# Kernel optimization log

Measured on AMD Instinct MI355X. Metric: run time of the kernel, lower is better.

## Reference

```python
import jax, jax.numpy as jnp
import numpy as np

N = 100000
E = 1600000
D = 64
BETA = 1.0


def setup_inputs() -> dict:
    key = jax.random.key(0)
    ks = jax.random.split(key, 6)
    x = jax.random.normal(ks[0], (N, D), dtype=jnp.float32)
    edge_index = jax.random.randint(ks[1], (2, E), 0, N, dtype=jnp.int64)
    s = 1.0 / np.sqrt(D)
    Wm = jax.random.uniform(ks[2], (D, D), jnp.float32, -s, s)
    bm = jax.random.uniform(ks[3], (D,), jnp.float32, -s, s)
    Wr = jax.random.uniform(ks[4], (D, D), jnp.float32, -s, s)
    br = jax.random.uniform(ks[5], (D,), jnp.float32, -s, s)
    return {"x": x, "edge_index": edge_index, "Wm": Wm, "bm": bm, "Wr": Wr, "br": br}


def reference(x, edge_index, Wm, bm, Wr, br):
    row, col = edge_index[0], edge_index[1]
    # gather source features and apply message linear: [E, D]
    messages = x[row] @ Wm + bm
    scores = BETA * messages.mean(axis=-1)  # [E]
    # edge softmax over incoming edges of each destination node (col)
    seg_max = jax.ops.segment_max(scores, col, num_segments=N)  # [N]
    ex = jnp.exp(scores - seg_max[col])  # [E]
    seg_sum = jax.ops.segment_sum(ex, col, num_segments=N)  # [N]
    weights = ex / seg_sum[col]  # [E]
    # weighted scatter-add back to destinations
    out = jax.ops.segment_sum(messages * weights[:, None], col, num_segments=N)
    return out + (x @ Wr + br)
```

## Files before the change

kernel.cpp:

```cpp
#include <hip/hip_runtime.h>
#include <math.h>

#define N_NODES 100000
#define DIM 64
#define N_EDGES 1600000

#define NBF 782
#define BK_NODES 128
#define CAP 3072

#define SC_CHUNK 8192
#define SC_BLOCKS ((N_EDGES + SC_CHUNK - 1) / SC_CHUNK)

#define HB 128
#define LIN_BLOCKS 1563
#define P1_BLOCKS (HB + LIN_BLOCKS)

typedef _Float16 half8 __attribute__((ext_vector_type(8)));
typedef _Float16 half4 __attribute__((ext_vector_type(4)));
typedef float f32x4 __attribute__((ext_vector_type(4)));

__global__ __launch_bounds__(256) void k_phase1(
        const float* __restrict__ x,
        const float* __restrict__ Wm, const float* __restrict__ bm,
        const float* __restrict__ Wr, const float* __restrict__ br,
        const int* __restrict__ col, int* __restrict__ hist,
        _Float16* __restrict__ Mh, float* __restrict__ es,
        float* __restrict__ out) {
    __shared__ int cnt[NBF];
    if (blockIdx.x < HB) {
        for (int i = threadIdx.x; i < NBF; i += 256) cnt[i] = 0;
        __syncthreads();
        for (int e = blockIdx.x * 256 + threadIdx.x; e < N_EDGES; e += HB * 256)
            atomicAdd(&cnt[col[e] >> 7], 1);
        __syncthreads();
        for (int i = threadIdx.x; i < NBF; i += 256)
            if (cnt[i]) atomicAdd(&hist[i], cnt[i]);
        return;
    }

    const int wave = (blockIdx.x - HB) * 4 + (threadIdx.x >> 6);
    if (wave >= N_NODES / 16) return;
    const int lane = threadIdx.x & 63;
    const int quad = lane >> 4;
    const int l15 = lane & 15;
    const int row0 = wave * 16;

    half8 bfrag[8][2];
#pragma unroll
    for (int ct = 0; ct < 8; ++ct) {
        const float* W = (ct < 4) ? Wm : Wr;
        const int c = (ct & 3) * 16 + l15;
#pragma unroll
        for (int kc = 0; kc < 2; ++kc) {
            half8 f;
#pragma unroll
            for (int j = 0; j < 8; ++j)
                f[j] = (_Float16)W[(kc * 32 + quad * 8 + j) * DIM + c];
            bfrag[ct][kc] = f;
        }
    }

    half8 afrag[2];
#pragma unroll
    for (int kc = 0; kc < 2; ++kc) {
        const float* xp = x + (size_t)(row0 + l15) * DIM + kc * 32 + quad * 8;
        const float4 x0 = *(const float4*)xp;
        const float4 x1 = *(const float4*)(xp + 4);
        half8 f;
        f[0] = (_Float16)x0.x; f[1] = (_Float16)x0.y;
        f[2] = (_Float16)x0.z; f[3] = (_Float16)x0.w;
        f[4] = (_Float16)x1.x; f[5] = (_Float16)x1.y;
        f[6] = (_Float16)x1.z; f[7] = (_Float16)x1.w;
        afrag[kc] = f;
    }

    f32x4 acc[8];
#pragma unroll
    for (int ct = 0; ct < 8; ++ct) {
        f32x4 a = {0.f, 0.f, 0.f, 0.f};
        a = __builtin_amdgcn_mfma_f32_16x16x32_f16(afrag[0], bfrag[ct][0], a, 0, 0, 0);
        a = __builtin_amdgcn_mfma_f32_16x16x32_f16(afrag[1], bfrag[ct][1], a, 0, 0, 0);
        acc[ct] = a;
    }

    float rsum[4] = {0.f, 0.f, 0.f, 0.f};
#pragma unroll
    for (int ct = 0; ct < 8; ++ct) {
        const float bias = (ct < 4) ? bm[(ct & 3) * 16 + l15]
                                    : br[(ct & 3) * 16 + l15];
#pragma unroll
        for (int r = 0; r < 4; ++r) {
            const float v = acc[ct][r] + bias;
            const size_t idx = (size_t)(row0 + quad * 4 + r) * DIM + (ct & 3) * 16 + l15;
            if (ct < 4) {
                Mh[idx] = (_Float16)v;
                rsum[r] += v;
            } else {
                out[idx] = v;
            }
        }
    }
#pragma unroll
    for (int o = 1; o <= 8; o <<= 1) {
#pragma unroll
        for (int r = 0; r < 4; ++r) rsum[r] += __shfl_xor(rsum[r], o, 64);
    }
    if (l15 == 0) {
#pragma unroll
        for (int r = 0; r < 4; ++r)
            es[row0 + quad * 4 + r] = __expf(rsum[r] * (1.0f / DIM));
    }
}


__global__ __launch_bounds__(1024) void k_scatter(
        const int* __restrict__ row, const int* __restrict__ col,
        int* __restrict__ cursor, unsigned int* __restrict__ pairs) {
    __shared__ int cnt[NBF];
    __shared__ int base_l[NBF];
    __shared__ int base_g[NBF];
    __shared__ int sd[1024];
    __shared__ unsigned int stage[SC_CHUNK];
    __shared__ unsigned short stage_bk[SC_CHUNK];

    const int t = threadIdx.x;
    const int start = blockIdx.x * SC_CHUNK;
    const int mEnd = min(N_EDGES, start + SC_CHUNK);

    for (int i = t; i < NBF; i += 1024) cnt[i] = 0;
    __syncthreads();

    int rr[8], cc[8], lr[8];
#pragma unroll
    for (int k = 0; k < 8; ++k) {
        const int idx = start + k * 1024 + t;
        if (idx < mEnd) {
            cc[k] = col[idx];
            rr[k] = row[idx];
            lr[k] = atomicAdd(&cnt[cc[k] >> 7], 1);
        }
    }
    __syncthreads();

    const int v = (t < NBF) ? cnt[t] : 0;
    sd[t] = v;
    __syncthreads();
    for (int o = 1; o < 1024; o <<= 1) {
        const int add = (t >= o) ? sd[t - o] : 0;
        __syncthreads();
        sd[t] += add;
        __syncthreads();
    }
    if (t < NBF) {
        base_l[t] = sd[t] - v;
        if (v > 0) base_g[t] = atomicAdd(&cursor[t], v);
    }
    __syncthreads();

#pragma unroll
    for (int k = 0; k < 8; ++k) {
        const int idx = start + k * 1024 + t;
        if (idx < mEnd) {
            const int bk = cc[k] >> 7;
            const int slot = base_l[bk] + lr[k];
            stage[slot] = ((unsigned int)rr[k] << 7) | (unsigned int)(cc[k] & 127);
            stage_bk[slot] = (unsigned short)bk;
        }
    }
    __syncthreads();

    const int m = mEnd - start;
    for (int i = t; i < m; i += 1024) {
        const int bk = stage_bk[i];
        const int gslot = base_g[bk] + (i - base_l[bk]);
        if (gslot < CAP) pairs[(size_t)bk * CAP + gslot] = stage[i];
    }
}

__global__ __launch_bounds__(512) void k_bucket_gather(
        const unsigned int* __restrict__ pairs, const int* __restrict__ cursor,
        const float* __restrict__ es, const half4* __restrict__ Mh4,
        float4* __restrict__ out4) {
    __shared__ unsigned int sorted[CAP];
    __shared__ int cnt[BK_NODES];
    __shared__ int off[BK_NODES];
    const int b = blockIdx.x;
    const int t = threadIdx.x;
    const int m = min(cursor[b], CAP);
    const size_t base = (size_t)b * CAP;

    if (t < BK_NODES) cnt[t] = 0;
    __syncthreads();

    unsigned int pk[6];
    int rk[6];
#pragma unroll
    for (int k = 0; k < 6; ++k) {
        const int i = k * 512 + t;
        if (i < m) {
            pk[k] = pairs[base + i];
            rk[k] = atomicAdd(&cnt[pk[k] & 127u], 1);
        }
    }
    __syncthreads();

    int v = 0;
    if (t < BK_NODES) {
        v = cnt[t];
        off[t] = v;
    }
    __syncthreads();
    for (int o = 1; o < BK_NODES; o <<= 1) {
        int add = 0;
        if (t < BK_NODES && t >= o) add = off[t - o];
        __syncthreads();
        if (t < BK_NODES) off[t] += add;
        __syncthreads();
    }
    if (t < BK_NODES) off[t] -= v;
    __syncthreads();

#pragma unroll
    for (int k = 0; k < 6; ++k) {
        const int i = k * 512 + t;
        if (i < m) sorted[off[pk[k] & 127u] + rk[k]] = pk[k];
    }
    __syncthreads();

    const int g = t >> 4;
    const int gl = t & 15;
    for (int c = g; c < BK_NODES; c += 32) {
        const int node = b * BK_NODES + c;
        if (node >= N_NODES) break;
        const int s0i = off[c];
        const int len = cnt[c];
        if (len == 0) continue;

        float a0x = 0.f, a0y = 0.f, a0z = 0.f, a0w = 0.f, l0 = 0.f;
        float a1x = 0.f, a1y = 0.f, a1z = 0.f, a1w = 0.f, l1 = 0.f;
        int j = 0;
        for (; j + 1 < len; j += 2) {
            const int s0 = (int)(sorted[s0i + j] >> 7);
            const int s1 = (int)(sorted[s0i + j + 1] >> 7);
            const float w0 = es[s0];
            const float w1 = es[s1];
            const half4 m0 = Mh4[(size_t)s0 * 16 + gl];
            const half4 m1 = Mh4[(size_t)s1 * 16 + gl];
            l0 += w0; l1 += w1;
            a0x = fmaf(w0, (float)m0[0], a0x); a0y = fmaf(w0, (float)m0[1], a0y);
            a0z = fmaf(w0, (float)m0[2], a0z); a0w = fmaf(w0, (float)m0[3], a0w);
            a1x = fmaf(w1, (float)m1[0], a1x); a1y = fmaf(w1, (float)m1[1], a1y);
            a1z = fmaf(w1, (float)m1[2], a1z); a1w = fmaf(w1, (float)m1[3], a1w);
        }
        if (j < len) {
            const int s0 = (int)(sorted[s0i + j] >> 7);
            const float w0 = es[s0];
            const half4 m0 = Mh4[(size_t)s0 * 16 + gl];
            l0 += w0;
            a0x = fmaf(w0, (float)m0[0], a0x); a0y = fmaf(w0, (float)m0[1], a0y);
            a0z = fmaf(w0, (float)m0[2], a0z); a0w = fmaf(w0, (float)m0[3], a0w);
        }
        const float inv = 1.0f / (l0 + l1);
        float4 r = out4[(size_t)node * 16 + gl];
        r.x = fmaf(a0x + a1x, inv, r.x);
        r.y = fmaf(a0y + a1y, inv, r.y);
        r.z = fmaf(a0z + a1z, inv, r.z);
        r.w = fmaf(a0w + a1w, inv, r.w);
        out4[(size_t)node * 16 + gl] = r;
    }
}

extern "C" void kernel_launch(void* const* d_in, const int* in_sizes, int n_in,
                              void* d_out, int out_size, void* d_ws, size_t ws_size,
                              hipStream_t stream) {
    const float* x  = (const float*)d_in[0];
    const int*   ei = (const int*)d_in[1];
    const float* Wm = (const float*)d_in[2];
    const float* bm = (const float*)d_in[3];
    const float* Wr = (const float*)d_in[4];
    const float* br = (const float*)d_in[5];
    float* out = (float*)d_out;
    const int* row = ei;
    const int* col = ei + N_EDGES;

    char* ws = (char*)d_ws;
    _Float16* Mh    = (_Float16*)ws;     ws += (size_t)N_NODES * DIM * sizeof(_Float16);
    float* es       = (float*)ws;        ws += (size_t)N_NODES * sizeof(float);
    int* hist       = (int*)ws;          ws += (size_t)1024 * sizeof(int);
    int* cursor     = (int*)ws;          ws += (size_t)1024 * sizeof(int);
    unsigned int* pairs = (unsigned int*)ws; ws += (size_t)NBF * CAP * sizeof(unsigned int);

    hipMemsetAsync(cursor, 0, NBF * sizeof(int), stream);

    k_phase1<<<P1_BLOCKS, 256, 0, stream>>>(x, Wm, bm, Wr, br,
                                            col, hist, Mh, es, out);
    k_scatter<<<SC_BLOCKS, 1024, 0, stream>>>(row, col, cursor, pairs);
    k_bucket_gather<<<NBF, 512, 0, stream>>>(pairs, cursor, es,
                                             (const half4*)Mh, (float4*)out);
}
```

Baseline: 164.7 us.

## Fuse edge scatter into GEMM phase kernel and drop unused histogram

Merges the edge bucket-scatter kernel into the node GEMM kernel as extra blocks of a single launch, so the scatter and the dense transform run at the same time and one launch is removed. The unused histogram pass is deleted. The shared-memory prefix scan is replaced by a wave-shuffle scan, which cuts the number of barriers. GEMM blocks now run 16 waves at 1024 threads and carry the large shared-memory footprint of the scatter path, which may lower occupancy for the GEMM part.

After: 157.3 us. -4.5%, faster.

```diff
diff --git a/kernel.cpp b/kernel.cpp
--- a/kernel.cpp
+++ b/kernel.cpp
@@ -12,36 +12,100 @@
 #define SC_CHUNK 8192
 #define SC_BLOCKS ((N_EDGES + SC_CHUNK - 1) / SC_CHUNK)
 
-#define HB 128
-#define LIN_BLOCKS 1563
-#define P1_BLOCKS (HB + LIN_BLOCKS)
+#define GEMM_BLOCKS ((N_NODES / 16 + 15) / 16)
+#define PH_BLOCKS (SC_BLOCKS + GEMM_BLOCKS)
 
 typedef _Float16 half8 __attribute__((ext_vector_type(8)));
 typedef _Float16 half4 __attribute__((ext_vector_type(4)));
 typedef float f32x4 __attribute__((ext_vector_type(4)));
 
-__global__ __launch_bounds__(256) void k_phase1(
+__global__ __launch_bounds__(1024) void k_phase(
         const float* __restrict__ x,
         const float* __restrict__ Wm, const float* __restrict__ bm,
         const float* __restrict__ Wr, const float* __restrict__ br,
-        const int* __restrict__ col, int* __restrict__ hist,
+        const int* __restrict__ row, const int* __restrict__ col,
+        int* __restrict__ cursor, unsigned int* __restrict__ pairs,
         _Float16* __restrict__ Mh, float* __restrict__ es,
         float* __restrict__ out) {
     __shared__ int cnt[NBF];
-    if (blockIdx.x < HB) {
-        for (int i = threadIdx.x; i < NBF; i += 256) cnt[i] = 0;
-        __syncthreads();
-        for (int e = blockIdx.x * 256 + threadIdx.x; e < N_EDGES; e += HB * 256)
-            atomicAdd(&cnt[col[e] >> 7], 1);
-        __syncthreads();
-        for (int i = threadIdx.x; i < NBF; i += 256)
-            if (cnt[i]) atomicAdd(&hist[i], cnt[i]);
+    __shared__ int base_l[NBF];
+    __shared__ int base_g[NBF];
+    __shared__ int wsum[16];
+    __shared__ unsigned int stage[SC_CHUNK];
+    __shared__ unsigned short stage_bk[SC_CHUNK];
+
+    const int t = threadIdx.x;
+    const int lane = t & 63;
+    const int wid = t >> 6;
+
+    if (blockIdx.x < SC_BLOCKS) {
+        const int start = blockIdx.x * SC_CHUNK;
+        const int mEnd = min(N_EDGES, start + SC_CHUNK);
+
+        for (int i = t; i < NBF; i += 1024) cnt[i] = 0;
+        __syncthreads();
+
+        int rr[8], cc[8], lr[8];
+#pragma unroll
+        for (int k = 0; k < 8; ++k) {
+            const int idx = start + k * 1024 + t;
+            if (idx < mEnd) {
+                cc[k] = col[idx];
+                rr[k] = row[idx];
+                lr[k] = atomicAdd(&cnt[cc[k] >> 7], 1);
+            }
+        }
+        __syncthreads();
+
+        const int v = (t < NBF) ? cnt[t] : 0;
+        int inc = v;
+#pragma unroll
+        for (int o = 1; o < 64; o <<= 1) {
+            const int u = __shfl_up(inc, o, 64);
+            if (lane >= o) inc += u;
+        }
+        if (lane == 63) wsum[wid] = inc;
+        __syncthreads();
+        if (wid == 0) {
+            const int wv = (lane < 16) ? wsum[lane] : 0;
+            int winc = wv;
+#pragma unroll
+            for (int o = 1; o < 16; o <<= 1) {
+                const int u = __shfl_up(winc, o, 64);
+                if (lane >= o) winc += u;
+            }
+            if (lane < 16) wsum[lane] = winc - wv;
+        }
+        __syncthreads();
+        if (t < NBF) {
+            base_l[t] = inc - v + wsum[wid];
+            if (v > 0) base_g[t] = atomicAdd(&cursor[t], v);
+        }
+        __syncthreads();
+
+#pragma unroll
+        for (int k = 0; k < 8; ++k) {
+            const int idx = start + k * 1024 + t;
+            if (idx < mEnd) {
+                const int bk = cc[k] >> 7;
+                const int slot = base_l[bk] + lr[k];
+                stage[slot] = ((unsigned int)rr[k] << 7) | (unsigned int)(cc[k] & 127);
+                stage_bk[slot] = (unsigned short)bk;
+            }
+        }
+        __syncthreads();
+
+        const int m = mEnd - start;
+        for (int i = t; i < m; i += 1024) {
+            const int bk = stage_bk[i];
+            const int gslot = base_g[bk] + (i - base_l[bk]);
+            if (gslot < CAP) pairs[(size_t)bk * CAP + gslot] = stage[i];
+        }
         return;
     }
 
-    const int wave = (blockIdx.x - HB) * 4 + (threadIdx.x >> 6);
+    const int wave = (blockIdx.x - SC_BLOCKS) * 16 + wid;
     if (wave >= N_NODES / 16) return;
-    const int lane = threadIdx.x & 63;
     const int quad = lane >> 4;
     const int l15 = lane & 15;
     const int row0 = wave * 16;
@@ -110,71 +174,6 @@
 #pragma unroll
         for (int r = 0; r < 4; ++r)
             es[row0 + quad * 4 + r] = __expf(rsum[r] * (1.0f / DIM));
-    }
-}
-
-
-__global__ __launch_bounds__(1024) void k_scatter(
-        const int* __restrict__ row, const int* __restrict__ col,
-        int* __restrict__ cursor, unsigned int* __restrict__ pairs) {
-    __shared__ int cnt[NBF];
-    __shared__ int base_l[NBF];
-    __shared__ int base_g[NBF];
-    __shared__ int sd[1024];
-    __shared__ unsigned int stage[SC_CHUNK];
-    __shared__ unsigned short stage_bk[SC_CHUNK];
-
-    const int t = threadIdx.x;
-    const int start = blockIdx.x * SC_CHUNK;
-    const int mEnd = min(N_EDGES, start + SC_CHUNK);
-
-    for (int i = t; i < NBF; i += 1024) cnt[i] = 0;
-    __syncthreads();
-
-    int rr[8], cc[8], lr[8];
-#pragma unroll
-    for (int k = 0; k < 8; ++k) {
-        const int idx = start + k * 1024 + t;
-        if (idx < mEnd) {
-            cc[k] = col[idx];
-            rr[k] = row[idx];
-            lr[k] = atomicAdd(&cnt[cc[k] >> 7], 1);
-        }
-    }
-    __syncthreads();
-
-    const int v = (t < NBF) ? cnt[t] : 0;
-    sd[t] = v;
-    __syncthreads();
-    for (int o = 1; o < 1024; o <<= 1) {
-        const int add = (t >= o) ? sd[t - o] : 0;
-        __syncthreads();
-        sd[t] += add;
-        __syncthreads();
-    }
-    if (t < NBF) {
-        base_l[t] = sd[t] - v;
-        if (v > 0) base_g[t] = atomicAdd(&cursor[t], v);
-    }
-    __syncthreads();
-
-#pragma unroll
-    for (int k = 0; k < 8; ++k) {
-        const int idx = start + k * 1024 + t;
-        if (idx < mEnd) {
-            const int bk = cc[k] >> 7;
-            const int slot = base_l[bk] + lr[k];
-            stage[slot] = ((unsigned int)rr[k] << 7) | (unsigned int)(cc[k] & 127);
-            stage_bk[slot] = (unsigned short)bk;
-        }
-    }
-    __syncthreads();
-
-    const int m = mEnd - start;
-    for (int i = t; i < m; i += 1024) {
-        const int bk = stage_bk[i];
-        const int gslot = base_g[bk] + (i - base_l[bk]);
-        if (gslot < CAP) pairs[(size_t)bk * CAP + gslot] = stage[i];
     }
 }
 
@@ -287,15 +286,13 @@
     char* ws = (char*)d_ws;
     _Float16* Mh    = (_Float16*)ws;     ws += (size_t)N_NODES * DIM * sizeof(_Float16);
     float* es       = (float*)ws;        ws += (size_t)N_NODES * sizeof(float);
-    int* hist       = (int*)ws;          ws += (size_t)1024 * sizeof(int);
     int* cursor     = (int*)ws;          ws += (size_t)1024 * sizeof(int);
     unsigned int* pairs = (unsigned int*)ws; ws += (size_t)NBF * CAP * sizeof(unsigned int);
 
     hipMemsetAsync(cursor, 0, NBF * sizeof(int), stream);
 
-    k_phase1<<<P1_BLOCKS, 256, 0, stream>>>(x, Wm, bm, Wr, br,
-                                            col, hist, Mh, es, out);
-    k_scatter<<<SC_BLOCKS, 1024, 0, stream>>>(row, col, cursor, pairs);
+    k_phase<<<PH_BLOCKS, 1024, 0, stream>>>(x, Wm, bm, Wr, br, row, col,
+                                            cursor, pairs, Mh, es, out);
     k_bucket_gather<<<NBF, 512, 0, stream>>>(pairs, cursor, es,
                                              (const half4*)Mh, (float4*)out);
 }
```
